# Performance work log

Measured on AMD Instinct MI355X. Metric: run time of the kernel, lower is better.

## Reference

```python
import jax, jax.numpy as jnp
import numpy as np

N, D, H, F = 50000, 128, 8, 512
HD = D // H
EPS_BN = 1e-5


def _batchnorm(x, gamma, beta):
    # BatchNorm1d in training mode: per-feature batch stats over node dim
    m = x.mean(axis=0)
    v = x.var(axis=0)
    return (x - m) * jax.lax.rsqrt(v + EPS_BN) * gamma + beta


def setup_inputs() -> dict:
    key = jax.random.key(0)
    ks = jax.random.split(key, 12)
    s = 0.05
    return {
        "src": jax.random.normal(ks[0], (N, D), jnp.float32),
        "edge_index": jax.random.randint(ks[1], (2, 800000), 0, N, jnp.int64),
        "q_w": jax.random.normal(ks[2], (D, D), jnp.float32) * s,
        "q_b": jnp.zeros((D,), jnp.float32),
        "k_w": jax.random.normal(ks[3], (D, D), jnp.float32) * s,
        "v_w": jax.random.normal(ks[4], (D, D), jnp.float32) * s,
        "out_w": jax.random.normal(ks[5], (D, D), jnp.float32) * s,
        "out_b": jnp.zeros((D,), jnp.float32),
        "g1": jnp.ones((D,), jnp.float32),
        "b1": jnp.zeros((D,), jnp.float32),
        "lin1_w": jax.random.normal(ks[6], (F, D), jnp.float32) * s,
        "lin1_b": jnp.zeros((F,), jnp.float32),
        "lin2_w": jax.random.normal(ks[7], (D, F), jnp.float32) * s,
        "lin2_b": jnp.zeros((D,), jnp.float32),
        "g2": jnp.ones((D,), jnp.float32),
        "b2": jnp.zeros((D,), jnp.float32),
    }


def reference(src, edge_index, q_w, q_b, k_w, v_w, out_w, out_b,
              g1, b1, lin1_w, lin1_b, lin2_w, lin2_b, g2, b2):
    n = src.shape[0]
    # add self loops, then attention edge index is (dst=edge[1], src=edge[0])
    loops = jnp.arange(n, dtype=edge_index.dtype)
    ei = jnp.concatenate([edge_index, jnp.stack([loops, loops])], axis=1)
    e_src, e_dst = ei[0], ei[1]  # message flows e_src -> e_dst; query index = e_dst

    scaling = float(HD) ** (-0.5)
    q = ((src @ q_w.T + q_b) * scaling).reshape(n, H, HD)
    k = (src @ k_w.T).reshape(n, H, HD)
    v = (src @ v_w.T).reshape(n, H, HD)

    # per-edge scores [E, H]
    w = jnp.einsum("ehd,ehd->eh", q[e_dst], k[e_src])
    # deterministic segment softmax over edges grouped by destination node
    mx = jax.ops.segment_max(w, e_dst, num_segments=n)
    ex = jnp.exp(w - mx[e_dst])
    den = jax.ops.segment_sum(ex, e_dst, num_segments=n)
    attn_w = ex / (den[e_dst] + 1e-16)  # [E, H]

    # weighted scatter-add aggregation -> [n, H, HD]
    msgs = attn_w[:, :, None] * v[e_src]
    agg = jax.ops.segment_sum(msgs, e_dst, num_segments=n)

    attn_out = agg.reshape(n, D) @ out_w.T + out_b
    x = _batchnorm(src + attn_out, g1, b1)

    ff = jax.nn.leaky_relu(x @ lin1_w.T + lin1_b, negative_slope=0.01)
    ff = ff @ lin2_w.T + lin2_b
    x = _batchnorm(x + ff, g2, b2)
    return x
```

## Files before the change

kernel.cpp:

```cpp
#include <hip/hip_runtime.h>
#include <math.h>

#define D 128
#define H 8
#define HD 16

typedef __attribute__((ext_vector_type(8))) short bf16x8;
typedef __attribute__((ext_vector_type(4))) float f32x4;

#define GLOBAL_AS __attribute__((address_space(1)))
#define LDS_AS    __attribute__((address_space(3)))

__device__ __forceinline__ ushort f2bf(float x) {
    union { float f; unsigned u; } v; v.f = x;
    unsigned r = v.u + 0x7fffu + ((v.u >> 16) & 1u);
    return (ushort)(r >> 16);
}
__device__ __forceinline__ float bflo(unsigned u) {
    union { unsigned u; float f; } x; x.u = u << 16; return x.f;
}
__device__ __forceinline__ float bfhi(unsigned u) {
    union { unsigned u; float f; } x; x.u = u & 0xffff0000u; return x.f;
}
__device__ __forceinline__ float bf2f(short s) {
    union { unsigned u; float f; } x; x.u = ((unsigned)(ushort)s) << 16; return x.f;
}

__device__ __forceinline__ float dot16(const float* qf, uint4 a, uint4 b) {
    float w;
    w  = qf[0]  * bflo(a.x) + qf[1]  * bfhi(a.x);
    w += qf[2]  * bflo(a.y) + qf[3]  * bfhi(a.y);
    w += qf[4]  * bflo(a.z) + qf[5]  * bfhi(a.z);
    w += qf[6]  * bflo(a.w) + qf[7]  * bfhi(a.w);
    w += qf[8]  * bflo(b.x) + qf[9]  * bfhi(b.x);
    w += qf[10] * bflo(b.y) + qf[11] * bfhi(b.y);
    w += qf[12] * bflo(b.z) + qf[13] * bfhi(b.z);
    w += qf[14] * bflo(b.w) + qf[15] * bfhi(b.w);
    return w;
}
__device__ __forceinline__ void acc16(float* num, float e, uint4 a, uint4 b) {
    num[0]  = fmaf(e, bflo(a.x), num[0]);  num[1]  = fmaf(e, bfhi(a.x), num[1]);
    num[2]  = fmaf(e, bflo(a.y), num[2]);  num[3]  = fmaf(e, bfhi(a.y), num[3]);
    num[4]  = fmaf(e, bflo(a.z), num[4]);  num[5]  = fmaf(e, bfhi(a.z), num[5]);
    num[6]  = fmaf(e, bflo(a.w), num[6]);  num[7]  = fmaf(e, bfhi(a.w), num[7]);
    num[8]  = fmaf(e, bflo(b.x), num[8]);  num[9]  = fmaf(e, bfhi(b.x), num[9]);
    num[10] = fmaf(e, bflo(b.y), num[10]); num[11] = fmaf(e, bfhi(b.y), num[11]);
    num[12] = fmaf(e, bflo(b.z), num[12]); num[13] = fmaf(e, bfhi(b.z), num[13]);
    num[14] = fmaf(e, bflo(b.w), num[14]); num[15] = fmaf(e, bfhi(b.w), num[15]);
}

template<int EPI, int M, int STATS>
__global__ __launch_bounds__(256)
void gemm_v4_kernel(const ushort* __restrict__ A,
                    const ushort* __restrict__ W,
                    const float* __restrict__ bias,
                    const float* __restrict__ extf,
                    ushort* __restrict__ outb,
                    float* __restrict__ stats,
                    int N)
{
    const int lane = threadIdx.x & 63, wave = threadIdx.x >> 6;
    const int lr = lane & 15, lq = lane >> 4;
    const int colbase = blockIdx.y * 128 + wave * 32;

    bf16x8 bfr[2][4];
    {
        const ushort* wp = W + (size_t)(colbase + lr) * 128 + lq * 8;
        #pragma unroll
        for (int ct = 0; ct < 2; ++ct)
            #pragma unroll
            for (int t = 0; t < 4; ++t)
                bfr[ct][t] = *(const bf16x8*)(wp + (size_t)ct * 16 * 128 + t * 32);
    }
    float biasv[2];
    biasv[0] = bias[colbase + lr];
    biasv[1] = bias[colbase + 16 + lr];

    float ssum[2] = {0.f, 0.f}, ssq[2] = {0.f, 0.f};

    const int stride = gridDim.x * 32;
    int r0 = blockIdx.x * 32;
    if (r0 < N) {
        bf16x8 cur[2][4], nxt[2][4];
        auto loadA = [&](int rb, bf16x8 (&dst)[2][4]) {
            #pragma unroll
            for (int s = 0; s < 2; ++s) {
                int ar = min(rb + s * 16 + lr, N - 1);
                const ushort* ap = A + (size_t)ar * 128 + lq * 8;
                #pragma unroll
                for (int t = 0; t < 4; ++t)
                    dst[s][t] = *(const bf16x8*)(ap + t * 32);
            }
        };
        loadA(r0, cur);

        while (true) {
            int rn = r0 + stride;
            if (rn < N) loadA(rn, nxt);

            f32x4 acc[2][2] = {};
            #pragma unroll
            for (int t = 0; t < 4; ++t) {
                acc[0][0] = __builtin_amdgcn_mfma_f32_16x16x32_bf16(cur[0][t], bfr[0][t], acc[0][0], 0, 0, 0);
                acc[1][0] = __builtin_amdgcn_mfma_f32_16x16x32_bf16(cur[1][t], bfr[0][t], acc[1][0], 0, 0, 0);
                acc[0][1] = __builtin_amdgcn_mfma_f32_16x16x32_bf16(cur[0][t], bfr[1][t], acc[0][1], 0, 0, 0);
                acc[1][1] = __builtin_amdgcn_mfma_f32_16x16x32_bf16(cur[1][t], bfr[1][t], acc[1][1], 0, 0, 0);
            }

            #pragma unroll
            for (int ct = 0; ct < 2; ++ct) {
                int gcol = colbase + ct * 16 + lr;
                #pragma unroll
                for (int s = 0; s < 2; ++s) {
                    #pragma unroll
                    for (int r = 0; r < 4; ++r) {
                        int grow = r0 + s * 16 + lq * 4 + r;
                        if (grow >= N) continue;
                        size_t o = (size_t)grow * M + gcol;
                        float v = acc[s][ct][r] + biasv[ct];
                        if (EPI == 2)      v = v > 0.f ? v : 0.01f * v;
                        else if (EPI == 3) v += extf[o];
                        if (STATS) { ssum[ct] += v; ssq[ct] = fmaf(v, v, ssq[ct]); }
                        outb[o] = f2bf(v);
                    }
                }
            }

            if (rn >= N) break;
            r0 = rn;
            #pragma unroll
            for (int s = 0; s < 2; ++s)
                #pragma unroll
                for (int t = 0; t < 4; ++t) cur[s][t] = nxt[s][t];
        }
    }

    if (STATS) {
        #pragma unroll
        for (int ct = 0; ct < 2; ++ct) {
            float a = ssum[ct], b = ssq[ct];
            a += __shfl_xor(a, 16, 64);  b += __shfl_xor(b, 16, 64);
            a += __shfl_xor(a, 32, 64);  b += __shfl_xor(b, 32, 64);
            if (lq == 0) {
                unsafeAtomicAdd(&stats[colbase + ct * 16 + lr], a);
                unsafeAtomicAdd(&stats[128 + colbase + ct * 16 + lr], b);
            }
        }
    }
}

__global__ __launch_bounds__(256)
void lin2_v6_kernel(const ushort* __restrict__ Ap,
                    const ushort* __restrict__ W,
                    const float* __restrict__ bias,
                    const ushort* __restrict__ extb,
                    const float* __restrict__ rawstats,
                    const float* __restrict__ gg,
                    const float* __restrict__ bb,
                    ushort* __restrict__ outb,
                    int N)
{
    constexpr int K = 512;
    __shared__ ushort alds[32 * K];

    const int lane = threadIdx.x & 63, wave = threadIdx.x >> 6;
    const int lr = lane & 15, lq = lane >> 4;
    const int row0 = blockIdx.x * 32;
    const int c0w  = wave * 32;

    #pragma unroll
    for (int i = 0; i < 8; ++i) {
        int r = wave * 8 + i;
        int gr = min(row0 + r, N - 1);
        const ushort* gsrc = Ap + (size_t)gr * K + (size_t)((lane ^ (r & 7)) * 8);
        __builtin_amdgcn_global_load_lds(
            (const GLOBAL_AS void*)gsrc,
            (LDS_AS void*)(alds + (size_t)r * K),
            16, 0, 0);
    }

    bf16x8 wA[8], wB[8];
    auto loadW = [&](int kc, bf16x8 (&wd)[8]) {
        const ushort* wp0 = W + (size_t)(c0w + lr) * K + kc * 128 + lq * 8;
        #pragma unroll
        for (int t = 0; t < 4; ++t) {
            wd[t]     = *(const bf16x8*)(wp0 + t * 32);
            wd[4 + t] = *(const bf16x8*)(wp0 + (size_t)16 * K + t * 32);
        }
    };
    loadW(0, wA);
    loadW(1, wB);

    __syncthreads();

    f32x4 acc[2][2] = {};
    bf16x8 a[2][4];
    auto ldsA = [&](int kc) {
        #pragma unroll
        for (int s = 0; s < 2; ++s) {
            const ushort* lp = alds + (size_t)(s * 16 + lr) * K;
            #pragma unroll
            for (int t = 0; t < 4; ++t)
                a[s][t] = *(const bf16x8*)(lp + (kc * 16 + ((t * 4 + lq) ^ (lr & 7))) * 8);
        }
    };
    auto mf = [&](bf16x8 (&wd)[8]) {
        #pragma unroll
        for (int t = 0; t < 4; ++t) {
            acc[0][0] = __builtin_amdgcn_mfma_f32_16x16x32_bf16(a[0][t], wd[t],     acc[0][0], 0, 0, 0);
            acc[1][0] = __builtin_amdgcn_mfma_f32_16x16x32_bf16(a[1][t], wd[t],     acc[1][0], 0, 0, 0);
            acc[0][1] = __builtin_amdgcn_mfma_f32_16x16x32_bf16(a[0][t], wd[4 + t], acc[0][1], 0, 0, 0);
            acc[1][1] = __builtin_amdgcn_mfma_f32_16x16x32_bf16(a[1][t], wd[4 + t], acc[1][1], 0, 0, 0);
        }
    };

    ldsA(0); mf(wA);
    loadW(2, wA);
    ldsA(1); mf(wB);
    loadW(3, wB);
    ldsA(2); mf(wA);
    ldsA(3); mf(wB);

    #pragma unroll
    for (int ct = 0; ct < 2; ++ct) {
        int col = c0w + ct * 16 + lr;
        float biasv = bias[col];
        float mean = rawstats[col] / (float)N;
        float var  = rawstats[128 + col] / (float)N - mean * mean;
        float scv = gg[col] * rsqrtf(var + 1e-5f);
        float shv = bb[col] - mean * scv;
        #pragma unroll
        for (int s = 0; s < 2; ++s) {
            #pragma unroll
            for (int r = 0; r < 4; ++r) {
                int grow = row0 + s * 16 + lq * 4 + r;
                if (grow >= N) continue;
                size_t o = (size_t)grow * 128 + col;
                float v = acc[s][ct][r] + biasv + fmaf(bf2f((short)extb[o]), scv, shv);
                outb[o] = f2bf(v);
            }
        }
    }
}

__global__ __launch_bounds__(256)
void convert_deg_kernel(const float* __restrict__ qw, const float* __restrict__ qb,
                        const float* __restrict__ kw, const float* __restrict__ vw,
                        const float* __restrict__ ow, const float* __restrict__ w1,
                        const float* __restrict__ w2,
                        ushort* __restrict__ wqkv, ushort* __restrict__ wout,
                        ushort* __restrict__ w1b, ushort* __restrict__ w2b,
                        float* __restrict__ bqkv,
                        const float* __restrict__ src, ushort* __restrict__ srcbf,
                        int nd8,
                        const int* __restrict__ ei, long long E0,
                        int* __restrict__ deg)
{
    long long i = (long long)blockIdx.x * 256 + threadIdx.x;
    if (i < E0) atomicAdd(&deg[ei[E0 + i]], 1);
    if (i < nd8) {
        const float4* sp = (const float4*)(src + i * 8);
        float4 f0 = sp[0], f1 = sp[1];
        ushort u[8];
        u[0]=f2bf(f0.x); u[1]=f2bf(f0.y); u[2]=f2bf(f0.z); u[3]=f2bf(f0.w);
        u[4]=f2bf(f1.x); u[5]=f2bf(f1.y); u[6]=f2bf(f1.z); u[7]=f2bf(f1.w);
        *(uint4*)(srcbf + i * 8) = *(uint4*)u;
    }
    if (i < 49152) {
        int row = (int)i >> 7;
        float v;
        if (row < 128)      v = 0.25f * qw[i];
        else if (row < 256) v = kw[i - 16384];
        else                v = vw[i - 32768];
        wqkv[i] = f2bf(v);
        return;
    }
    long long j = i - 49152;
    if (j < 16384) { wout[j] = f2bf(ow[j]); return; }
    j -= 16384;
    if (j < 65536) { w1b[j] = f2bf(w1[j]); return; }
    j -= 65536;
    if (j < 65536) { w2b[j] = f2bf(w2[j]); return; }
    j -= 65536;
    if (j < 384) bqkv[j] = (j < 128) ? 0.25f * qb[j] : 0.f;
}

__global__ __launch_bounds__(256)
void w1fold_kernel(const ushort* __restrict__ w1b, const float* __restrict__ lb1,
                   const float* __restrict__ rawstats,
                   const float* __restrict__ g1, const float* __restrict__ b1,
                   ushort* __restrict__ w1f, float* __restrict__ bias1f, int N)
{
    int f = blockIdx.x * 4 + (threadIdx.x >> 6);
    int lane = threadIdx.x & 63;
    int k0 = lane * 2;
    float m0 = rawstats[k0] / (float)N;
    float v0 = rawstats[128 + k0] / (float)N - m0 * m0;
    float sc0 = g1[k0] * rsqrtf(v0 + 1e-5f);
    float sh0 = b1[k0] - m0 * sc0;
    float m1 = rawstats[k0 + 1] / (float)N;
    float v1 = rawstats[128 + k0 + 1] / (float)N - m1 * m1;
    float sc1 = g1[k0 + 1] * rsqrtf(v1 + 1e-5f);
    float sh1 = b1[k0 + 1] - m1 * sc1;

    uint wp = *(const uint*)(w1b + (size_t)f * 128 + k0);
    float w0 = bflo(wp), w1v = bfhi(wp);
    uint o = (uint)f2bf(w0 * sc0) | ((uint)f2bf(w1v * sc1) << 16);
    *(uint*)(w1f + (size_t)f * 128 + k0) = o;

    float part = w0 * sh0 + w1v * sh1;
    #pragma unroll
    for (int m = 1; m < 64; m <<= 1) part += __shfl_xor(part, m, 64);
    if (lane == 0) bias1f[f] = lb1[f] + part;
}

__global__ __launch_bounds__(256)
void scan_block_sum(const int* __restrict__ deg, int n, int* __restrict__ bsum)
{
    __shared__ int sh[256];
    int i = blockIdx.x * 256 + threadIdx.x;
    sh[threadIdx.x] = (i < n) ? deg[i] : 0;
    __syncthreads();
    for (int ofs = 128; ofs > 0; ofs >>= 1) {
        if (threadIdx.x < ofs) sh[threadIdx.x] += sh[threadIdx.x + ofs];
        __syncthreads();
    }
    if (threadIdx.x == 0) bsum[blockIdx.x] = sh[0];
}

__global__ __launch_bounds__(256)
void scan_final(const int* __restrict__ deg, int n, const int* __restrict__ bsum,
                int nb, int* __restrict__ rowptr)
{
    __shared__ int sb[256];
    __shared__ int sh[256];
    int t = threadIdx.x;
    sb[t] = (t < nb) ? bsum[t] : 0;
    __syncthreads();
    for (int ofs = 1; ofs < 256; ofs <<= 1) {
        int v = (t >= ofs) ? sb[t - ofs] : 0;
        __syncthreads();
        sb[t] += v;
        __syncthreads();
    }
    int boff = (blockIdx.x == 0) ? 0 : sb[blockIdx.x - 1];

    int i = blockIdx.x * 256 + t;
    int v = (i < n) ? deg[i] : 0;
    sh[t] = v;
    __syncthreads();
    for (int ofs = 1; ofs < 256; ofs <<= 1) {
        int u = (t >= ofs) ? sh[t - ofs] : 0;
        __syncthreads();
        sh[t] += u;
        __syncthreads();
    }
    if (i < n) rowptr[i] = boff + sh[t] - v;
    if (i == n - 1) rowptr[n] = boff + sh[t];
}

__global__ __launch_bounds__(256)
void scatter_kernel(const int* __restrict__ ei, long long E0,
                    const int* __restrict__ rowptr, int* __restrict__ cnt,
                    int* __restrict__ col)
{
    long long e = (long long)blockIdx.x * 256 + threadIdx.x;
    if (e >= E0) return;
    int s = ei[e], d = ei[E0 + e];
    int pos = rowptr[d] + atomicAdd(&cnt[d], 1);
    col[pos] = s;
}

__global__ __launch_bounds__(256)
void gat_agg_kernel(const int* __restrict__ rowptr, const int* __restrict__ col,
                    const ushort* __restrict__ qkv, ushort* __restrict__ agg, int N)
{
    int node = blockIdx.x * 4 + (threadIdx.x >> 6);
    if (node >= N) return;
    int lane = threadIdx.x & 63;
    int es = lane >> 3, h = lane & 7;
    const uint4* Q = (const uint4*)qkv;

    const uint4* qp = Q + (size_t)node * 48 + h * 2;
    uint4 qa = qp[0], qb = qp[1];
    float qf[16];
    qf[0]=bflo(qa.x); qf[1]=bfhi(qa.x); qf[2]=bflo(qa.y); qf[3]=bfhi(qa.y);
    qf[4]=bflo(qa.z); qf[5]=bfhi(qa.z); qf[6]=bflo(qa.w); qf[7]=bfhi(qa.w);
    qf[8]=bflo(qb.x); qf[9]=bfhi(qb.x); qf[10]=bflo(qb.y); qf[11]=bfhi(qb.y);
    qf[12]=bflo(qb.z); qf[13]=bfhi(qb.z); qf[14]=bflo(qb.w); qf[15]=bfhi(qb.w);

    float num[16];
    #pragma unroll
    for (int i = 0; i < 16; i++) num[i] = 0.f;
    float den = 0.f;

    int beg = rowptr[node];
    int total = rowptr[node + 1] - beg + 1;

    int idx = es;
    if (idx < total) {
        int s0 = (idx == 0) ? node : col[beg + idx - 1];
        const uint4* rp0 = Q + (size_t)s0 * 48 + h * 2;
        uint4 ka = rp0[16], kb = rp0[17], va = rp0[32], vb = rp0[33];
        int idx1 = idx + 8;
        int s1 = (idx1 < total) ? col[beg + idx1 - 1] : 0;

        while (true) {
            bool more = idx1 < total;
            uint4 ka1, kb1, va1, vb1;
            if (more) {
                const uint4* rp1 = Q + (size_t)s1 * 48 + h * 2;
                ka1 = rp1[16]; kb1 = rp1[17]; va1 = rp1[32]; vb1 = rp1[33];
            }
            int idx2 = idx1 + 8;
            int s2 = (idx2 < total) ? col[beg + idx2 - 1] : 0;

            float ev = __expf(dot16(qf, ka, kb));
            den += ev;
            acc16(num, ev, va, vb);

            if (!more) break;
            ka = ka1; kb = kb1; va = va1; vb = vb1;
            s1 = s2; idx1 = idx2;
        }
    }

    #pragma unroll
    for (int m = 8; m < 64; m <<= 1) {
        den += __shfl_xor(den, m, 64);
        #pragma unroll
        for (int i = 0; i < 16; i++) num[i] += __shfl_xor(num[i], m, 64);
    }

    if (es == 0) {
        float inv = 1.f / (den + 1e-16f);
        uint4 o0, o1;
        o0.x = (uint)f2bf(num[0]*inv)  | ((uint)f2bf(num[1]*inv)  << 16);
        o0.y = (uint)f2bf(num[2]*inv)  | ((uint)f2bf(num[3]*inv)  << 16);
        o0.z = (uint)f2bf(num[4]*inv)  | ((uint)f2bf(num[5]*inv)  << 16);
        o0.w = (uint)f2bf(num[6]*inv)  | ((uint)f2bf(num[7]*inv)  << 16);
        o1.x = (uint)f2bf(num[8]*inv)  | ((uint)f2bf(num[9]*inv)  << 16);
        o1.y = (uint)f2bf(num[10]*inv) | ((uint)f2bf(num[11]*inv) << 16);
        o1.z = (uint)f2bf(num[12]*inv) | ((uint)f2bf(num[13]*inv) << 16);
        o1.w = (uint)f2bf(num[14]*inv) | ((uint)f2bf(num[15]*inv) << 16);
        uint4* op = (uint4*)(agg + (size_t)node * 128 + h * 16);
        op[0] = o0; op[1] = o1;
    }
}

__global__ __launch_bounds__(256)
void bn_stats_bf16_kernel(const ushort* __restrict__ y, int N, float* __restrict__ stats)
{
    int jp = threadIdx.x & 63;
    int q4 = threadIdx.x >> 6;
    int r = blockIdx.x * 256 + q4;
    int rend = min(N, (int)(blockIdx.x + 1) * 256);
    float s0 = 0.f, qq0 = 0.f, s1 = 0.f, qq1 = 0.f;
    const uint* yp = (const uint*)y;
    for (; r < rend; r += 4) {
        uint u = yp[(size_t)r * 64 + jp];
        float a = bflo(u), b = bfhi(u);
        s0 += a; qq0 += a * a; s1 += b; qq1 += b * b;
    }
    __shared__ float sh[4][64][4];
    sh[q4][jp][0] = s0; sh[q4][jp][1] = qq0; sh[q4][jp][2] = s1; sh[q4][jp][3] = qq1;
    __syncthreads();
    if (threadIdx.x < 128) {
        int p = threadIdx.x >> 1;
        int w = threadIdx.x & 1;
        float ss = 0.f, sq = 0.f;
        #pragma unroll
        for (int i = 0; i < 4; i++) { ss += sh[i][p][w * 2]; sq += sh[i][p][w * 2 + 1]; }
        unsafeAtomicAdd(&stats[2 * p + w], ss);
        unsafeAtomicAdd(&stats[128 + 2 * p + w], sq);
    }
}

__global__ __launch_bounds__(256)
void bn_apply_out_kernel(const ushort* __restrict__ y, const float* __restrict__ rawstats,
                         const float* __restrict__ g, const float* __restrict__ b,
                         float* __restrict__ out, int total4, int N)
{
    __shared__ float scs[128], shs[128];
    if (threadIdx.x < 128) {
        int j = threadIdx.x;
        float mean = rawstats[j] / (float)N;
        float var  = rawstats[128 + j] / (float)N - mean * mean;
        float sc = g[j] * rsqrtf(var + 1e-5f);
        scs[j] = sc;
        shs[j] = b[j] - mean * sc;
    }
    __syncthreads();
    int i = blockIdx.x * 256 + threadIdx.x;
    if (i >= total4) return;
    uint2 u = reinterpret_cast<const uint2*>(y)[i];
    int j = (i * 4) & (D - 1);
    float4 v;
    v.x = bflo(u.x) * scs[j + 0] + shs[j + 0];
    v.y = bfhi(u.x) * scs[j + 1] + shs[j + 1];
    v.z = bflo(u.y) * scs[j + 2] + shs[j + 2];
    v.w = bfhi(u.y) * scs[j + 3] + shs[j + 3];
    reinterpret_cast<float4*>(out)[i] = v;
}

extern "C" void kernel_launch(void* const* d_in, const int* in_sizes, int n_in,
                              void* d_out, int out_size, void* d_ws, size_t ws_size,
                              hipStream_t stream)
{
    const float* src    = (const float*)d_in[0];
    const int*   ei     = (const int*)  d_in[1];
    const float* q_w    = (const float*)d_in[2];
    const float* q_b    = (const float*)d_in[3];
    const float* k_w    = (const float*)d_in[4];
    const float* v_w    = (const float*)d_in[5];
    const float* out_w  = (const float*)d_in[6];
    const float* out_b  = (const float*)d_in[7];
    const float* g1     = (const float*)d_in[8];
    const float* b1     = (const float*)d_in[9];
    const float* lin1_w = (const float*)d_in[10];
    const float* lin1_b = (const float*)d_in[11];
    const float* lin2_w = (const float*)d_in[12];
    const float* lin2_b = (const float*)d_in[13];
    const float* g2     = (const float*)d_in[14];
    const float* b2     = (const float*)d_in[15];

    const int N        = in_sizes[0] / D;
    const long long E0 = in_sizes[1] / 2;

    float* ws = (float*)d_ws;
    size_t off = 0;
    ushort* qkv   = (ushort*)(ws + off); off += (size_t)N * 192;
    ushort* agg   = (ushort*)(ws + off); off += (size_t)N * 64;
    ushort* srcbf = (ushort*)(ws + off); off += (size_t)N * 64;
    ushort* y1b   = (ushort*)(ws + off); off += (size_t)N * 64;
    ushort* hid   = (ushort*)(ws + off); off += (size_t)N * 256;
    ushort* y2b   = (ushort*)(ws + off); off += (size_t)N * 64;
    ushort* wqkv  = (ushort*)(ws + off); off += 24576;
    ushort* woutb = (ushort*)(ws + off); off += 8192;
    ushort* w1b   = (ushort*)(ws + off); off += 32768;
    ushort* w1f   = (ushort*)(ws + off); off += 32768;
    ushort* w2b   = (ushort*)(ws + off); off += 32768;
    float*  bqkv  = ws + off;            off += 384;
    float*  bias1f= ws + off;            off += 512;
    size_t zero_start = off;
    int* deg    = (int*)(ws + off); off += N;
    int* cnt    = (int*)(ws + off); off += N;
    float* stats1 = ws + off; off += 512;
    float* stats2 = ws + off; off += 512;
    size_t zero_cnt = off - zero_start;
    int* rowptr = (int*)(ws + off); off += N + 1;
    int* bsum   = (int*)(ws + off); off += 256;
    int* col    = (int*)(ws + off); off += E0;

    hipMemsetAsync(ws + zero_start, 0, zero_cnt * sizeof(float), stream);

    dim3 blk(256);

    dim3 gE0((unsigned)((E0 + 255) / 256));
    hipLaunchKernelGGL(convert_deg_kernel, gE0, blk, 0, stream,
                       q_w, q_b, k_w, v_w, out_w, lin1_w, lin2_w,
                       wqkv, woutb, w1b, w2b, bqkv,
                       src, srcbf, N * 16, ei, E0, deg);

    int nb = (N + 255) / 256;
    hipLaunchKernelGGL(scan_block_sum, dim3(nb), blk, 0, stream, deg, N, bsum);
    hipLaunchKernelGGL(scan_final, dim3(nb), blk, 0, stream, deg, N, bsum, nb, rowptr);
    hipLaunchKernelGGL(scatter_kernel, gE0, blk, 0, stream, ei, E0, rowptr, cnt, col);

    const int gx = 1024;

    hipLaunchKernelGGL((gemm_v4_kernel<0, 384, 0>), dim3(gx, 3), blk, 0, stream,
                       srcbf, wqkv, bqkv, nullptr, qkv, nullptr, N);

    hipLaunchKernelGGL(gat_agg_kernel, dim3((N + 3) / 4), blk, 0, stream,
                       rowptr, col, qkv, agg, N);

    hipLaunchKernelGGL((gemm_v4_kernel<3, 128, 1>), dim3(gx, 1), blk, 0, stream,
                       agg, woutb, out_b, src, y1b, stats1, N);

    hipLaunchKernelGGL(w1fold_kernel, dim3(128), blk, 0, stream,
                       w1b, lin1_b, stats1, g1, b1, w1f, bias1f, N);

    hipLaunchKernelGGL((gemm_v4_kernel<2, 512, 0>), dim3(gx, 4), blk, 0, stream,
                       y1b, w1f, bias1f, nullptr, hid, nullptr, N);

    hipLaunchKernelGGL(lin2_v6_kernel, dim3((N + 31) / 32), blk, 0, stream,
                       hid, w2b, lin2_b, y1b, stats1, g1, b1, y2b, N);

    dim3 gS((N + 255) / 256);
    hipLaunchKernelGGL(bn_stats_bf16_kernel, gS, blk, 0, stream, y2b, N, stats2);
    int total4 = N * D / 4;
    hipLaunchKernelGGL(bn_apply_out_kernel, dim3((total4 + 255) / 256), blk, 0, stream,
                       y2b, stats2, g2, b2, (float*)d_out, total4, N);
}
```

Baseline: 424.5 us.

## Stage GEMM A tiles into swizzled double-buffered LDS via direct global-to-LDS loads

The bf16 GEMM kernel no longer has each wave load the whole 32x128 A tile into its own registers. The block now loads the tile once into a double-buffered LDS array using global_load_lds, with an XOR swizzle on 16-byte chunks, and the MFMA operands are read back from LDS. This removes the four-fold duplicate global/L2 reads of A across waves and lowers register pressure from the register prefetch buffers. In exchange it adds a per-iteration block barrier, depends on the async LDS loads being complete at that barrier, and uses 16 KB of LDS per block.

```diff
diff --git a/kernel.cpp b/kernel.cpp
--- a/kernel.cpp
+++ b/kernel.cpp
@@ -51,7 +51,7 @@
 
 template<int EPI, int M, int STATS>
 __global__ __launch_bounds__(256)
-void gemm_v4_kernel(const ushort* __restrict__ A,
+void gemm_v7_kernel(const ushort* __restrict__ A,
                     const ushort* __restrict__ W,
                     const float* __restrict__ bias,
                     const float* __restrict__ extf,
@@ -59,6 +59,8 @@
                     float* __restrict__ stats,
                     int N)
 {
+    __shared__ ushort alds[2][32 * 128];
+
     const int lane = threadIdx.x & 63, wave = threadIdx.x >> 6;
     const int lr = lane & 15, lq = lane >> 4;
     const int colbase = blockIdx.y * 128 + wave * 32;
@@ -78,61 +80,71 @@
 
     float ssum[2] = {0.f, 0.f}, ssq[2] = {0.f, 0.f};
 
+    auto stage = [&](int rb, int b) {
+        #pragma unroll
+        for (int i = 0; i < 2; ++i) {
+            int r = wave * 8 + i * 4 + (lane >> 4);
+            int gr = min(rb + r, N - 1);
+            int c = (lane & 15) ^ (r & 7);
+            __builtin_amdgcn_global_load_lds(
+                (const GLOBAL_AS void*)(A + (size_t)gr * 128 + c * 8),
+                (LDS_AS void*)(&alds[b][(wave * 8 + i * 4) * 128]),
+                16, 0, 0);
+        }
+    };
+
     const int stride = gridDim.x * 32;
     int r0 = blockIdx.x * 32;
-    if (r0 < N) {
-        bf16x8 cur[2][4], nxt[2][4];
-        auto loadA = [&](int rb, bf16x8 (&dst)[2][4]) {
+
+    stage(r0, 0);
+    __syncthreads();
+    int cur = 0;
+
+    while (true) {
+        int rn = r0 + stride;
+        if (rn < N) stage(rn, cur ^ 1);
+
+        bf16x8 a[2][4];
+        #pragma unroll
+        for (int s = 0; s < 2; ++s) {
+            const ushort* lp = &alds[cur][(s * 16 + lr) * 128];
+            #pragma unroll
+            for (int t = 0; t < 4; ++t)
+                a[s][t] = *(const bf16x8*)(lp + ((t * 4 + lq) ^ (lr & 7)) * 8);
+        }
+
+        f32x4 acc[2][2] = {};
+        #pragma unroll
+        for (int t = 0; t < 4; ++t) {
+            acc[0][0] = __builtin_amdgcn_mfma_f32_16x16x32_bf16(a[0][t], bfr[0][t], acc[0][0], 0, 0, 0);
+            acc[1][0] = __builtin_amdgcn_mfma_f32_16x16x32_bf16(a[1][t], bfr[0][t], acc[1][0], 0, 0, 0);
+            acc[0][1] = __builtin_amdgcn_mfma_f32_16x16x32_bf16(a[0][t], bfr[1][t], acc[0][1], 0, 0, 0);
+            acc[1][1] = __builtin_amdgcn_mfma_f32_16x16x32_bf16(a[1][t], bfr[1][t], acc[1][1], 0, 0, 0);
+        }
+
+        #pragma unroll
+        for (int ct = 0; ct < 2; ++ct) {
+            int gcol = colbase + ct * 16 + lr;
             #pragma unroll
             for (int s = 0; s < 2; ++s) {
-                int ar = min(rb + s * 16 + lr, N - 1);
-                const ushort* ap = A + (size_t)ar * 128 + lq * 8;
                 #pragma unroll
-                for (int t = 0; t < 4; ++t)
-                    dst[s][t] = *(const bf16x8*)(ap + t * 32);
-            }
-        };
-        loadA(r0, cur);
-
-        while (true) {
-            int rn = r0 + stride;
-            if (rn < N) loadA(rn, nxt);
-
-            f32x4 acc[2][2] = {};
-            #pragma unroll
-            for (int t = 0; t < 4; ++t) {
-                acc[0][0] = __builtin_amdgcn_mfma_f32_16x16x32_bf16(cur[0][t], bfr[0][t], acc[0][0], 0, 0, 0);
-                acc[1][0] = __builtin_amdgcn_mfma_f32_16x16x32_bf16(cur[1][t], bfr[0][t], acc[1][0], 0, 0, 0);
-                acc[0][1] = __builtin_amdgcn_mfma_f32_16x16x32_bf16(cur[0][t], bfr[1][t], acc[0][1], 0, 0, 0);
-                acc[1][1] = __builtin_amdgcn_mfma_f32_16x16x32_bf16(cur[1][t], bfr[1][t], acc[1][1], 0, 0, 0);
-            }
-
-            #pragma unroll
-            for (int ct = 0; ct < 2; ++ct) {
-                int gcol = colbase + ct * 16 + lr;
-                #pragma unroll
-                for (int s = 0; s < 2; ++s) {
-                    #pragma unroll
-                    for (int r = 0; r < 4; ++r) {
-                        int grow = r0 + s * 16 + lq * 4 + r;
-                        if (grow >= N) continue;
-                        size_t o = (size_t)grow * M + gcol;
-                        float v = acc[s][ct][r] + biasv[ct];
-                        if (EPI == 2)      v = v > 0.f ? v : 0.01f * v;
-                        else if (EPI == 3) v += extf[o];
-                        if (STATS) { ssum[ct] += v; ssq[ct] = fmaf(v, v, ssq[ct]); }
-                        outb[o] = f2bf(v);
-                    }
+                for (int r = 0; r < 4; ++r) {
+                    int grow = r0 + s * 16 + lq * 4 + r;
+                    if (grow >= N) continue;
+                    size_t o = (size_t)grow * M + gcol;
+                    float v = acc[s][ct][r] + biasv[ct];
+                    if (EPI == 2)      v = v > 0.f ? v : 0.01f * v;
+                    else if (EPI == 3) v += extf[o];
+                    if (STATS) { ssum[ct] += v; ssq[ct] = fmaf(v, v, ssq[ct]); }
+                    outb[o] = f2bf(v);
                 }
             }
-
-            if (rn >= N) break;
-            r0 = rn;
-            #pragma unroll
-            for (int s = 0; s < 2; ++s)
-                #pragma unroll
-                for (int t = 0; t < 4; ++t) cur[s][t] = nxt[s][t];
-        }
+        }
+
+        if (rn >= N) break;
+        __syncthreads();
+        cur ^= 1;
+        r0 = rn;
     }
 
     if (STATS) {
@@ -569,19 +581,19 @@
 
     const int gx = 1024;
 
-    hipLaunchKernelGGL((gemm_v4_kernel<0, 384, 0>), dim3(gx, 3), blk, 0, stream,
+    hipLaunchKernelGGL((gemm_v7_kernel<0, 384, 0>), dim3(gx, 3), blk, 0, stream,
                        srcbf, wqkv, bqkv, nullptr, qkv, nullptr, N);
 
     hipLaunchKernelGGL(gat_agg_kernel, dim3((N + 3) / 4), blk, 0, stream,
                        rowptr, col, qkv, agg, N);
 
-    hipLaunchKernelGGL((gemm_v4_kernel<3, 128, 1>), dim3(gx, 1), blk, 0, stream,
+    hipLaunchKernelGGL((gemm_v7_kernel<3, 128, 1>), dim3(gx, 1), blk, 0, stream,
                        agg, woutb, out_b, src, y1b, stats1, N);
 
     hipLaunchKernelGGL(w1fold_kernel, dim3(128), blk, 0, stream,
                        w1b, lin1_b, stats1, g1, b1, w1f, bias1f, N);
 
-    hipLaunchKernelGGL((gemm_v4_kernel<2, 512, 0>), dim3(gx, 4), blk, 0, stream,
+    hipLaunchKernelGGL((gemm_v7_kernel<2, 512, 0>), dim3(gx, 4), blk, 0, stream,
                        y1b, w1f, bias1f, nullptr, hid, nullptr, N);
 
     hipLaunchKernelGGL(lin2_v6_kernel, dim3((N + 31) / 32), blk, 0, stream,
```

Measured after the change: 391.6 us, median of 3. 1.08x faster.
